# Kernel optimization log

Hardware: AMD Instinct MI355X
Metric: run time of the kernel (lower is better)

Reference implementation:

```python
import jax, jax.numpy as jnp
import numpy as np

B, C, T_IN = 32, 512, 1024
T_OUT = 4096  # fixed total expanded length (all rows of durations sum to this)


def setup_inputs() -> dict:
    key = jax.random.key(0)
    k_enc, k_cut = jax.random.split(key)
    encodings = jax.random.normal(k_enc, (B, C, T_IN), dtype=jnp.float32)
    # durations: nonnegative ints summing exactly to T_OUT per row, mean ~4.
    # Build as diffs of sorted random cut points in [0, T_OUT].
    cuts = jnp.sort(jax.random.randint(k_cut, (B, T_IN - 1), 0, T_OUT), axis=1)
    lo = jnp.zeros((B, 1), dtype=cuts.dtype)
    hi = jnp.full((B, 1), T_OUT, dtype=cuts.dtype)
    bounds = jnp.concatenate([lo, cuts, hi], axis=1)  # [B, T_IN+1]
    durations = (bounds[:, 1:] - bounds[:, :-1]).astype(jnp.int64)  # [B, T_IN]
    return {"encodings": encodings, "durations": durations}


def reference(encodings, durations):
    # Fused length regulation: instead of per-batch repeat_interleave + stack,
    # compute the gather index map from cumulative durations in one pass.
    # out[b, :, t] = encodings[b, :, j] where j = searchsorted(cumsum(dur[b]), t, 'right')
    cum = jnp.cumsum(durations, axis=1)  # [B, T_IN], last col == T_OUT
    t = jnp.arange(T_OUT)  # [T_OUT]
    idx = jax.vmap(lambda c: jnp.searchsorted(c, t, side="right"))(cum)  # [B, T_OUT]
    # gather along time axis, broadcast over channels
    return jnp.take_along_axis(encodings, idx[:, None, :], axis=2)  # [B, C, T_OUT]
```

## Files before the change

### kernel.cpp

```cpp
#include <hip/hip_runtime.h>
#include <hip/hip_bf16.h>

#define B_DIM 32
#define C_DIM 512
#define T_IN 1024
#define T_OUT 4096

__global__ __launch_bounds__(256) void build_idx_kernel(
    const int* __restrict__ dur, int* __restrict__ idx) {
    __shared__ int s_part[256];

    const int b = blockIdx.x;
    const int tid = threadIdx.x;

    int4 v = ((const int4*)(dur + b * T_IN))[tid];
    int local = v.x + v.y + v.z + v.w;

    s_part[tid] = local;
    __syncthreads();
    #pragma unroll
    for (int off = 1; off < 256; off <<= 1) {
        int val = s_part[tid];
        int add = (tid >= off) ? s_part[tid - off] : 0;
        __syncthreads();
        s_part[tid] = val + add;
        __syncthreads();
    }
    int start = s_part[tid] - local;

    int* row = idx + b * T_OUT;
    int j0 = tid * 4;
    #pragma unroll
    for (int k = 0; k < 4; ++k) {
        int dk = (k == 0) ? v.x : (k == 1) ? v.y : (k == 2) ? v.z : v.w;
        for (int r = 0; r < dk; ++r) {
            row[start + r] = j0 + k;
        }
        start += dk;
    }
}

__global__ __launch_bounds__(256) void gather_kernel(
    const float* __restrict__ enc, const int* __restrict__ idx,
    float* __restrict__ out) {
    __shared__ float s_row[T_IN];

    const int bc = blockIdx.x;
    const int b = bc >> 9;
    const int tid = threadIdx.x;

    ((float4*)s_row)[tid] = ((const float4*)(enc + (size_t)bc * T_IN))[tid];
    __syncthreads();

    const int4* idx_row = (const int4*)(idx + b * T_OUT);
    float4* out_row = (float4*)(out + (size_t)bc * T_OUT);

    #pragma unroll
    for (int g = 0; g < 4; ++g) {
        const int t4 = g * 256 + tid;
        int4 j = idx_row[t4];
        float4 o;
        o.x = s_row[j.x];
        o.y = s_row[j.y];
        o.z = s_row[j.z];
        o.w = s_row[j.w];
        out_row[t4] = o;
    }
}

extern "C" void kernel_launch(void* const* d_in, const int* in_sizes, int n_in,
                              void* d_out, int out_size, void* d_ws, size_t ws_size,
                              hipStream_t stream) {
    const float* enc = (const float*)d_in[0];
    const int* dur = (const int*)d_in[1];
    float* out = (float*)d_out;
    int* idx = (int*)d_ws;

    build_idx_kernel<<<B_DIM, 256, 0, stream>>>(dur, idx);
    gather_kernel<<<B_DIM * C_DIM, 256, 0, stream>>>(enc, idx, out);
}
```

Before: 320.6 us.

## Binary-search index build, multi-channel gather blocks, nontemporal loads and stores

```diff
diff --git a/kernel.cpp b/kernel.cpp
--- a/kernel.cpp
+++ b/kernel.cpp
@@ -5,18 +5,23 @@
 #define C_DIM 512
 #define T_IN 1024
 #define T_OUT 4096
+#define CPB 4
+
+typedef float nfloat4 __attribute__((ext_vector_type(4)));
+typedef int nint4 __attribute__((ext_vector_type(4)));
 
 __global__ __launch_bounds__(256) void build_idx_kernel(
     const int* __restrict__ dur, int* __restrict__ idx) {
+    __shared__ int s_cum[T_IN];
     __shared__ int s_part[256];
 
     const int b = blockIdx.x;
     const int tid = threadIdx.x;
 
-    int4 v = ((const int4*)(dur + b * T_IN))[tid];
-    int local = v.x + v.y + v.z + v.w;
+    nint4 v = ((const nint4*)(dur + b * T_IN))[tid];
+    int c1 = v.x, c2 = c1 + v.y, c3 = c2 + v.z, c4 = c3 + v.w;
 
-    s_part[tid] = local;
+    s_part[tid] = c4;
     __syncthreads();
     #pragma unroll
     for (int off = 1; off < 256; off <<= 1) {
@@ -26,45 +31,68 @@
         s_part[tid] = val + add;
         __syncthreads();
     }
-    int start = s_part[tid] - local;
+    int prefix = s_part[tid] - c4;
+
+    nint4 cumv;
+    cumv.x = prefix + c1;
+    cumv.y = prefix + c2;
+    cumv.z = prefix + c3;
+    cumv.w = prefix + c4;
+    ((nint4*)s_cum)[tid] = cumv;
+    __syncthreads();
 
     int* row = idx + b * T_OUT;
-    int j0 = tid * 4;
     #pragma unroll
-    for (int k = 0; k < 4; ++k) {
-        int dk = (k == 0) ? v.x : (k == 1) ? v.y : (k == 2) ? v.z : v.w;
-        for (int r = 0; r < dk; ++r) {
-            row[start + r] = j0 + k;
+    for (int k = 0; k < 16; ++k) {
+        const int t = k * 256 + tid;
+        int lo = 0, hi = T_IN - 1;
+        #pragma unroll
+        for (int s = 0; s < 10; ++s) {
+            int mid = (lo + hi) >> 1;
+            bool gt = s_cum[mid] > t;
+            hi = gt ? mid : hi;
+            lo = gt ? lo : mid + 1;
         }
-        start += dk;
+        row[t] = lo;
     }
 }
 
 __global__ __launch_bounds__(256) void gather_kernel(
     const float* __restrict__ enc, const int* __restrict__ idx,
     float* __restrict__ out) {
-    __shared__ float s_row[T_IN];
+    __shared__ float s_rows[CPB][T_IN];
 
-    const int bc = blockIdx.x;
-    const int b = bc >> 9;
+    const int blk = blockIdx.x;
+    const int b = blk >> 7;
+    const int c0 = (blk & 127) * CPB;
     const int tid = threadIdx.x;
 
-    ((float4*)s_row)[tid] = ((const float4*)(enc + (size_t)bc * T_IN))[tid];
+    const float* enc_base = enc + ((size_t)(b * C_DIM + c0)) * T_IN;
+    #pragma unroll
+    for (int cc = 0; cc < CPB; ++cc) {
+        nfloat4 v = __builtin_nontemporal_load(
+            ((const nfloat4*)(enc_base + cc * T_IN)) + tid);
+        ((nfloat4*)s_rows[cc])[tid] = v;
+    }
     __syncthreads();
 
-    const int4* idx_row = (const int4*)(idx + b * T_OUT);
-    float4* out_row = (float4*)(out + (size_t)bc * T_OUT);
+    const nint4* idx_row = (const nint4*)(idx + b * T_OUT);
+    float* out_base = out + ((size_t)(b * C_DIM + c0)) * T_OUT;
 
     #pragma unroll
     for (int g = 0; g < 4; ++g) {
         const int t4 = g * 256 + tid;
-        int4 j = idx_row[t4];
-        float4 o;
-        o.x = s_row[j.x];
-        o.y = s_row[j.y];
-        o.z = s_row[j.z];
-        o.w = s_row[j.w];
-        out_row[t4] = o;
+        nint4 j = idx_row[t4];
+        #pragma unroll
+        for (int cc = 0; cc < CPB; ++cc) {
+            nfloat4 o;
+            o.x = s_rows[cc][j.x];
+            o.y = s_rows[cc][j.y];
+            o.z = s_rows[cc][j.z];
+            o.w = s_rows[cc][j.w];
+            __builtin_nontemporal_store(
+                o, ((nfloat4*)(out_base + (size_t)cc * T_OUT)) + t4);
+        }
     }
 }
 
@@ -77,5 +105,5 @@
     int* idx = (int*)d_ws;
 
     build_idx_kernel<<<B_DIM, 256, 0, stream>>>(dur, idx);
-    gather_kernel<<<B_DIM * C_DIM, 256, 0, stream>>>(enc, idx, out);
+    gather_kernel<<<B_DIM * (C_DIM / CPB), 256, 0, stream>>>(enc, idx, out);
 }
```

New measurement: 312.4 us (median of 2 runs). 2.6% less time.
